# Optimization experiments

Measured on AMD Instinct MI355X. Metric: run time of the kernel, lower is better.

Reference implementation:

```python
import jax, jax.numpy as jnp
import numpy as np

B, S, D = 4, 4096, 2048
NUM_MODALITIES = 2


def setup_inputs() -> dict:
    key = jax.random.key(0)
    k_x, k_t, k_w0, k_b0, k_w1, k_b1 = jax.random.split(key, 6)
    scale = 1.0 / np.sqrt(D)
    return {
        "hidden_states": jax.random.normal(k_x, (B, S, D), dtype=jnp.float32),
        "type_ids": jax.random.randint(k_t, (B, S), 0, NUM_MODALITIES, dtype=jnp.int32),
        "W0": jax.random.uniform(k_w0, (D, D), jnp.float32, -scale, scale),
        "b0": jax.random.uniform(k_b0, (D,), jnp.float32, -scale, scale),
        "W1": jax.random.uniform(k_w1, (D, D), jnp.float32, -scale, scale),
        "b1": jax.random.uniform(k_b1, (D,), jnp.float32, -scale, scale),
    }


def reference(hidden_states, type_ids, W0, b0, W1, b1):
    # Original: gather tokens where type_ids == i, apply expert i's Linear,
    # scatter into a zero-init [B, S, out_dim] buffer. The masks partition
    # all tokens, so this equals a masked mixture of the two dense GEMMs.
    y0 = jnp.einsum("bsd,ed->bse", hidden_states, W0) + b0  # expert 0
    y1 = jnp.einsum("bsd,ed->bse", hidden_states, W1) + b1  # expert 1
    m0 = (type_ids == 0)[..., None]
    m1 = (type_ids == 1)[..., None]
    zero = jnp.zeros((), dtype=y0.dtype)
    return jnp.where(m0, y0, zero) + jnp.where(m1, y1, zero)
```

## Files before the change

kernel.cpp:

```cpp
#include <hip/hip_runtime.h>
#include <hip/hip_bf16.h>
#include <stdint.h>


#define T_TOK 16384
#define DDIM  2048
#define NT_K  32
#define NT_D  64
#define MT    64
#define NTILE 8

typedef __attribute__((ext_vector_type(4))) float          f32x4;
typedef __attribute__((ext_vector_type(8))) short          bf16x8;
typedef __attribute__((ext_vector_type(2))) unsigned int   u32x2;

#define WS_HBF   0ull
#define WS_W0BF  67108864ull
#define WS_W1BF  75497472ull
#define WS_META  83886080ull
#define WS_IDX   83886208ull
#define WS_NEED  (WS_IDX + 65536ull)

__device__ __forceinline__ unsigned short cvt1_bf16(float f) {
  unsigned u = __builtin_bit_cast(unsigned, f);
  unsigned rnd = 0x7fffu + ((u >> 16) & 1u);
  return (unsigned short)((u + rnd) >> 16);
}

__device__ __forceinline__ void gload_lds16(const void* g, void* l) {
  __builtin_amdgcn_global_load_lds(
      (const __attribute__((address_space(1))) unsigned int*)g,
      (__attribute__((address_space(3))) unsigned int*)l, 16, 0, 0);
}

#define BAR()     asm volatile("s_barrier" ::: "memory")
#define VMCNT2()  asm volatile("s_waitcnt vmcnt(2)" ::: "memory")
#define VMCNT4()  asm volatile("s_waitcnt vmcnt(4)" ::: "memory")
#define VMCNT0()  asm volatile("s_waitcnt vmcnt(0)" ::: "memory")
#define LGKM0()   asm volatile("s_waitcnt lgkmcnt(0)" ::: "memory")
#define SCHEDBAR() __builtin_amdgcn_sched_barrier(0)

__global__ void k_prep(const float* __restrict__ H, const float* __restrict__ W0,
                       const float* __restrict__ W1, const int* __restrict__ typ,
                       unsigned short* __restrict__ Hbf,
                       unsigned short* __restrict__ W0bf,
                       unsigned short* __restrict__ W1bf,
                       int* __restrict__ meta, int* __restrict__ idx) {
  const int gid = blockIdx.x * blockDim.x + threadIdx.x;
  if (gid < T_TOK) {
    int t = typ[gid];
    int pos = (t == 0) ? atomicAdd(&meta[0], 1)
                       : (T_TOK - 1) - atomicAdd(&meta[1], 1);
    idx[pos] = gid;
  }
  const int nH = T_TOK * DDIM / 4;
  const int nW = DDIM * DDIM / 4;
  const int total = nH + 2 * nW;
  const int stride = gridDim.x * blockDim.x;
  for (int i = gid; i < total; i += stride) {
    const float* s; unsigned short* d; int j;
    if (i < nH)           { s = H;  d = Hbf;  j = i; }
    else if (i < nH + nW) { s = W0; d = W0bf; j = i - nH; }
    else                  { s = W1; d = W1bf; j = i - nH - nW; }
    f32x4 v = ((const f32x4*)s)[j];
    unsigned p0 = (unsigned)cvt1_bf16(v[0]) | ((unsigned)cvt1_bf16(v[1]) << 16);
    unsigned p1 = (unsigned)cvt1_bf16(v[2]) | ((unsigned)cvt1_bf16(v[3]) << 16);
    u32x2 o; o[0] = p0; o[1] = p1;
    ((u32x2*)d)[j] = o;
  }
}

__global__ __launch_bounds__(512) void k_gemm256(
    const unsigned short* __restrict__ Hbf,
    const unsigned short* __restrict__ W0bf,
    const unsigned short* __restrict__ W1bf,
    const float* __restrict__ B0, const float* __restrict__ B1,
    const int* __restrict__ meta, const int* __restrict__ idx,
    float* __restrict__ OUT)
{
  __shared__ char lds[131072];

  const int orig = blockIdx.x;
  const int wg = (orig & 7) * 64 + (orig >> 3);
  int my = wg >> 3;
  const int bx = wg & 7;

  const int c0 = meta[0];
  int ms = c0 >> 8; if (ms > MT - 1) ms = MT - 1;
  my = (my == 0) ? ms : (my == ms) ? 0 : my;

  const int tid  = threadIdx.x;
  const int lane = tid & 63;
  const int wid  = tid >> 6;
  const int wr   = wid >> 2;
  const int wc   = wid & 3;
  const int fr   = lane & 15;
  const int g    = lane >> 4;

  const int start = my * 256;
  const int isDual = (start < c0 && c0 < start + 256) ? 1 : 0;
  const int e0    = (start >= c0) ? 1 : 0;
  const int colBase = bx * 256;

  const int cs = (lane & 3) ^ ((lane >> 3) & 3);
  const char* aS[2];
  int rt[2];
#pragma unroll
  for (int l = 0; l < 2; ++l) {
    int ch = 2 * wid + l;
    rt[l] = ch * 16 + (lane >> 2);
    int orow = idx[start + rt[l]];
    aS[l] = (const char*)Hbf + (size_t)orow * 4096 + cs * 16;
  }
  const int chB = (2 * wid) * 1024;

  const int sw = (g ^ ((fr >> 1) & 3)) << 4;
  int aF[8], bF[4];
#pragma unroll
  for (int m = 0; m < 8; ++m) aF[m] = ((wr * 128 + m * 16 + fr) << 6) + sw;
#pragma unroll
  for (int n = 0; n < 4; ++n) bF[n] = ((wc * 64 + n * 16 + fr) << 6) + sw;

  f32x4 acc[8][4];
#pragma unroll
  for (int m = 0; m < 8; ++m)
#pragma unroll
    for (int n = 0; n < 4; ++n) acc[m][n] = (f32x4)0.0f;

  int cols[4];
#pragma unroll
  for (int n = 0; n < 4; ++n) cols[n] = colBase + wc * 64 + n * 16 + fr;

  if (!isDual) {
    const unsigned short* Wb = e0 ? W1bf : W0bf;
    const char* wS[2];
#pragma unroll
    for (int l = 0; l < 2; ++l)
      wS[l] = (const char*)(Wb + (size_t)(colBase + rt[l]) * DDIM) + cs * 16;

    auto STAGE_A = [&](int d, int kh, int tn) {
      char* dst = lds + (d << 15) + (kh << 14) + chB;
      int ko = tn * 128 + kh * 64;
      gload_lds16(aS[0] + ko, dst);
      gload_lds16(aS[1] + ko, dst + 1024);
    };
    auto STAGE_B = [&](int d, int kh, int tn) {
      char* dst = lds + 65536 + (d << 15) + (kh << 14) + chB;
      int ko = tn * 128 + kh * 64;
      gload_lds16(wS[0] + ko, dst);
      gload_lds16(wS[1] + ko, dst + 1024);
    };

    STAGE_A(0, 0, 0); STAGE_B(0, 0, 0); STAGE_A(0, 1, 0); STAGE_B(0, 1, 0);
    VMCNT4();
    BAR();

#pragma unroll 2
    for (int t = 0; t < NT_K; ++t) {
      const int c = t & 1, d = c ^ 1;
      int t1 = t + 1; if (t1 == NT_K) t1 = NT_K - 1;
      const char* Ak0 = lds + (c << 15);
      const char* Ak1 = Ak0 + 16384;
      const char* Bk0 = lds + 65536 + (c << 15);
      const char* Bk1 = Bk0 + 16384;

      bf16x8 a[8], bb0, bb1;

#pragma unroll
      for (int m = 0; m < 8; ++m) a[m] = *(const bf16x8*)(Ak0 + aF[m]);
      bb0 = *(const bf16x8*)(Bk0 + bF[0]);
      bb1 = *(const bf16x8*)(Bk0 + bF[1]);
      STAGE_A(d, 0, t1);
      BAR(); LGKM0(); SCHEDBAR();
      __builtin_amdgcn_s_setprio(1);
#pragma unroll
      for (int m = 0; m < 8; ++m) {
        acc[m][0] = __builtin_amdgcn_mfma_f32_16x16x32_bf16(a[m], bb0, acc[m][0], 0, 0, 0);
        acc[m][1] = __builtin_amdgcn_mfma_f32_16x16x32_bf16(a[m], bb1, acc[m][1], 0, 0, 0);
      }
      __builtin_amdgcn_s_setprio(0);

      bb0 = *(const bf16x8*)(Bk0 + bF[2]);
      bb1 = *(const bf16x8*)(Bk0 + bF[3]);
      VMCNT2();
      STAGE_B(d, 0, t1);
      BAR(); LGKM0(); SCHEDBAR();
      __builtin_amdgcn_s_setprio(1);
#pragma unroll
      for (int m = 0; m < 8; ++m) {
        acc[m][2] = __builtin_amdgcn_mfma_f32_16x16x32_bf16(a[m], bb0, acc[m][2], 0, 0, 0);
        acc[m][3] = __builtin_amdgcn_mfma_f32_16x16x32_bf16(a[m], bb1, acc[m][3], 0, 0, 0);
      }
      __builtin_amdgcn_s_setprio(0);

#pragma unroll
      for (int m = 0; m < 8; ++m) a[m] = *(const bf16x8*)(Ak1 + aF[m]);
      bb0 = *(const bf16x8*)(Bk1 + bF[0]);
      bb1 = *(const bf16x8*)(Bk1 + bF[1]);
      STAGE_A(d, 1, t1);
      BAR(); LGKM0(); SCHEDBAR();
      __builtin_amdgcn_s_setprio(1);
#pragma unroll
      for (int m = 0; m < 8; ++m) {
        acc[m][0] = __builtin_amdgcn_mfma_f32_16x16x32_bf16(a[m], bb0, acc[m][0], 0, 0, 0);
        acc[m][1] = __builtin_amdgcn_mfma_f32_16x16x32_bf16(a[m], bb1, acc[m][1], 0, 0, 0);
      }
      __builtin_amdgcn_s_setprio(0);

      bb0 = *(const bf16x8*)(Bk1 + bF[2]);
      bb1 = *(const bf16x8*)(Bk1 + bF[3]);
      VMCNT2();
      STAGE_B(d, 1, t1);
      BAR(); LGKM0(); SCHEDBAR();
      __builtin_amdgcn_s_setprio(1);
#pragma unroll
      for (int m = 0; m < 8; ++m) {
        acc[m][2] = __builtin_amdgcn_mfma_f32_16x16x32_bf16(a[m], bb0, acc[m][2], 0, 0, 0);
        acc[m][3] = __builtin_amdgcn_mfma_f32_16x16x32_bf16(a[m], bb1, acc[m][3], 0, 0, 0);
      }
      __builtin_amdgcn_s_setprio(0);
    }

    VMCNT0();

    const float* Bv = e0 ? B1 : B0;
    float bias[4];
#pragma unroll
    for (int n = 0; n < 4; ++n) bias[n] = Bv[cols[n]];
#pragma unroll
    for (int m = 0; m < 8; ++m) {
      int lb = wr * 128 + m * 16 + (g << 2);
#pragma unroll
      for (int j = 0; j < 4; ++j) {
        int orow = idx[start + lb + j];
        float* op = OUT + (size_t)orow * DDIM;
#pragma unroll
        for (int n = 0; n < 4; ++n) op[cols[n]] = acc[m][n][j] + bias[n];
      }
    }
  } else {
    const char* wS0[2]; const char* wS1[2];
#pragma unroll
    for (int l = 0; l < 2; ++l) {
      wS0[l] = (const char*)(W0bf + (size_t)(colBase + rt[l]) * DDIM) + cs * 16;
      wS1[l] = (const char*)(W1bf + (size_t)(colBase + rt[l]) * DDIM) + cs * 16;
    }
    const int lo_w = c0 - start - wr * 128;
    int mmix = 8;
    if (lo_w > 0 && lo_w < 128 && (lo_w & 15)) mmix = lo_w >> 4;

    f32x4 accX[4];
#pragma unroll
    for (int n = 0; n < 4; ++n) accX[n] = (f32x4)0.0f;

    auto DSTAGE = [&](int d, int tn) {
      int ko = tn * 64;
      char* ad  = lds + (d << 14) + chB;
      char* b0d = lds + 32768 + (d << 14) + chB;
      char* b1d = lds + 65536 + (d << 14) + chB;
      gload_lds16(aS[0] + ko, ad);
      gload_lds16(aS[1] + ko, ad + 1024);
      gload_lds16(wS0[0] + ko, b0d);
      gload_lds16(wS0[1] + ko, b0d + 1024);
      gload_lds16(wS1[0] + ko, b1d);
      gload_lds16(wS1[1] + ko, b1d + 1024);
    };

    DSTAGE(0, 0);
    VMCNT0();
    BAR();

    for (int t = 0; t < NT_D; ++t) {
      const int c = t & 1, d = c ^ 1;
      int t1 = t + 1; if (t1 == NT_D) t1 = NT_D - 1;
      const char* Ac  = lds + (c << 14);
      const char* B0c = lds + 32768 + (c << 14);
      const char* B1c = lds + 65536 + (c << 14);
      bf16x8 a[8], b0a, b0b, b1a, b1b;

#pragma unroll
      for (int m = 0; m < 8; ++m) a[m] = *(const bf16x8*)(Ac + aF[m]);
      b0a = *(const bf16x8*)(B0c + bF[0]);
      b0b = *(const bf16x8*)(B0c + bF[1]);
      b1a = *(const bf16x8*)(B1c + bF[0]);
      b1b = *(const bf16x8*)(B1c + bF[1]);
      DSTAGE(d, t1);
      BAR(); LGKM0(); SCHEDBAR();
      __builtin_amdgcn_s_setprio(1);
#pragma unroll
      for (int m = 0; m < 8; ++m) {
        if (m == mmix) {
          acc[m][0] = __builtin_amdgcn_mfma_f32_16x16x32_bf16(a[m], b0a, acc[m][0], 0, 0, 0);
          acc[m][1] = __builtin_amdgcn_mfma_f32_16x16x32_bf16(a[m], b0b, acc[m][1], 0, 0, 0);
          accX[0]   = __builtin_amdgcn_mfma_f32_16x16x32_bf16(a[m], b1a, accX[0],   0, 0, 0);
          accX[1]   = __builtin_amdgcn_mfma_f32_16x16x32_bf16(a[m], b1b, accX[1],   0, 0, 0);
        } else if (m * 16 >= lo_w) {
          acc[m][0] = __builtin_amdgcn_mfma_f32_16x16x32_bf16(a[m], b1a, acc[m][0], 0, 0, 0);
          acc[m][1] = __builtin_amdgcn_mfma_f32_16x16x32_bf16(a[m], b1b, acc[m][1], 0, 0, 0);
        } else {
          acc[m][0] = __builtin_amdgcn_mfma_f32_16x16x32_bf16(a[m], b0a, acc[m][0], 0, 0, 0);
          acc[m][1] = __builtin_amdgcn_mfma_f32_16x16x32_bf16(a[m], b0b, acc[m][1], 0, 0, 0);
        }
      }
      __builtin_amdgcn_s_setprio(0);

      b0a = *(const bf16x8*)(B0c + bF[2]);
      b0b = *(const bf16x8*)(B0c + bF[3]);
      b1a = *(const bf16x8*)(B1c + bF[2]);
      b1b = *(const bf16x8*)(B1c + bF[3]);
      VMCNT0();
      BAR(); LGKM0(); SCHEDBAR();
      __builtin_amdgcn_s_setprio(1);
#pragma unroll
      for (int m = 0; m < 8; ++m) {
        if (m == mmix) {
          acc[m][2] = __builtin_amdgcn_mfma_f32_16x16x32_bf16(a[m], b0a, acc[m][2], 0, 0, 0);
          acc[m][3] = __builtin_amdgcn_mfma_f32_16x16x32_bf16(a[m], b0b, acc[m][3], 0, 0, 0);
          accX[2]   = __builtin_amdgcn_mfma_f32_16x16x32_bf16(a[m], b1a, accX[2],   0, 0, 0);
          accX[3]   = __builtin_amdgcn_mfma_f32_16x16x32_bf16(a[m], b1b, accX[3],   0, 0, 0);
        } else if (m * 16 >= lo_w) {
          acc[m][2] = __builtin_amdgcn_mfma_f32_16x16x32_bf16(a[m], b1a, acc[m][2], 0, 0, 0);
          acc[m][3] = __builtin_amdgcn_mfma_f32_16x16x32_bf16(a[m], b1b, acc[m][3], 0, 0, 0);
        } else {
          acc[m][2] = __builtin_amdgcn_mfma_f32_16x16x32_bf16(a[m], b0a, acc[m][2], 0, 0, 0);
          acc[m][3] = __builtin_amdgcn_mfma_f32_16x16x32_bf16(a[m], b0b, acc[m][3], 0, 0, 0);
        }
      }
      __builtin_amdgcn_s_setprio(0);
    }
    VMCNT0();

    float bias0v[4], bias1v[4];
#pragma unroll
    for (int n = 0; n < 4; ++n) { bias0v[n] = B0[cols[n]]; bias1v[n] = B1[cols[n]]; }
#pragma unroll
    for (int m = 0; m < 8; ++m) {
      int lb = wr * 128 + m * 16 + (g << 2);
      if (m == mmix) {
#pragma unroll
        for (int j = 0; j < 4; ++j) {
          int p = start + lb + j;
          int orow = idx[p];
          float* op = OUT + (size_t)orow * DDIM;
          if (p >= c0) {
#pragma unroll
            for (int n = 0; n < 4; ++n) op[cols[n]] = accX[n][j] + bias1v[n];
          } else {
#pragma unroll
            for (int n = 0; n < 4; ++n) op[cols[n]] = acc[m][n][j] + bias0v[n];
          }
        }
      } else {
        int em = (m * 16 >= lo_w) ? 1 : 0;
#pragma unroll
        for (int j = 0; j < 4; ++j) {
          int orow = idx[start + lb + j];
          float* op = OUT + (size_t)orow * DDIM;
#pragma unroll
          for (int n = 0; n < 4; ++n)
            op[cols[n]] = acc[m][n][j] + (em ? bias1v[n] : bias0v[n]);
        }
      }
    }
  }
}

#define BMd 64
#define BNd 64
#define BKd 32
#define LDW 36

__device__ __forceinline__ bf16x8 cvt_bf16x8(f32x4 lo, f32x4 hi) {
  bf16x8 r;
#pragma unroll
  for (int i = 0; i < 4; ++i) {
    r[i]     = (short)cvt1_bf16(lo[i]);
    r[i + 4] = (short)cvt1_bf16(hi[i]);
  }
  return r;
}

__global__ __launch_bounds__(256, 2) void mot_mfma_diag(
    const float* __restrict__ H,  const int* __restrict__ TYP,
    const float* __restrict__ W0, const float* __restrict__ B0,
    const float* __restrict__ W1, const float* __restrict__ B1,
    float* __restrict__ OUT)
{
  __shared__ float As[BMd * LDW];
  __shared__ float W0s[BNd * LDW];
  __shared__ float W1s[BNd * LDW];

  const int tid = threadIdx.x;
  const int rowBase = blockIdx.y * BMd;
  const int colBase = blockIdx.x * BNd;
  const int srow  = tid >> 3;
  const int scol4 = (tid & 7) << 2;
  const float* hA  = H  + (size_t)(rowBase + srow) * DDIM + scol4;
  const float* hW0 = W0 + (size_t)(colBase + srow) * DDIM + scol4;
  const float* hW1 = W1 + (size_t)(colBase + srow) * DDIM + scol4;

  const int lane = tid & 63;
  const int w    = tid >> 6;
  const int fr   = lane & 15;
  const int g    = lane >> 4;

  f32x4 acc0[4], acc1[4];
#pragma unroll
  for (int m = 0; m < 4; ++m) { acc0[m] = (f32x4)0.0f; acc1[m] = (f32x4)0.0f; }

  for (int k0 = 0; k0 < DDIM; k0 += BKd) {
    f32x4 va[2], v0[2], v1[2];
#pragma unroll
    for (int p = 0; p < 2; ++p) {
      va[p] = *(const f32x4*)(hA  + (size_t)p * 32 * DDIM);
      v0[p] = *(const f32x4*)(hW0 + (size_t)p * 32 * DDIM);
      v1[p] = *(const f32x4*)(hW1 + (size_t)p * 32 * DDIM);
    }
    hA += BKd; hW0 += BKd; hW1 += BKd;
    __syncthreads();
#pragma unroll
    for (int p = 0; p < 2; ++p) {
      int r = srow + 32 * p;
      *(f32x4*)(&As [r * LDW + scol4]) = va[p];
      *(f32x4*)(&W0s[r * LDW + scol4]) = v0[p];
      *(f32x4*)(&W1s[r * LDW + scol4]) = v1[p];
    }
    __syncthreads();

    bf16x8 af[4];
#pragma unroll
    for (int m = 0; m < 4; ++m) {
      const float* ap = &As[(m * 16 + fr) * LDW + g * 8];
      af[m] = cvt_bf16x8(*(const f32x4*)ap, *(const f32x4*)(ap + 4));
    }
    const float* b0p = &W0s[(w * 16 + fr) * LDW + g * 8];
    const float* b1p = &W1s[(w * 16 + fr) * LDW + g * 8];
    bf16x8 bf0 = cvt_bf16x8(*(const f32x4*)b0p, *(const f32x4*)(b0p + 4));
    bf16x8 bf1 = cvt_bf16x8(*(const f32x4*)b1p, *(const f32x4*)(b1p + 4));
#pragma unroll
    for (int m = 0; m < 4; ++m) {
      acc0[m] = __builtin_amdgcn_mfma_f32_16x16x32_bf16(af[m], bf0, acc0[m], 0, 0, 0);
      acc1[m] = __builtin_amdgcn_mfma_f32_16x16x32_bf16(af[m], bf1, acc1[m], 0, 0, 0);
    }
  }

  const int col = colBase + w * 16 + fr;
  const float bz0 = B0[col];
  const float bz1 = B1[col];
#pragma unroll
  for (int m = 0; m < 4; ++m)
#pragma unroll
    for (int j = 0; j < 4; ++j) {
      int row = rowBase + m * 16 + (g << 2) + j;
      int t = TYP[row];
      OUT[(size_t)row * DDIM + col] = (t == 0) ? (acc0[m][j] + bz0) : (acc1[m][j] + bz1);
    }
}

extern "C" void kernel_launch(void* const* d_in, const int* in_sizes, int n_in,
                              void* d_out, int out_size, void* d_ws, size_t ws_size,
                              hipStream_t stream) {
  const float* H   = (const float*)d_in[0];
  const int*   TYP = (const int*)  d_in[1];
  const float* W0  = (const float*)d_in[2];
  const float* B0v = (const float*)d_in[3];
  const float* W1  = (const float*)d_in[4];
  const float* B1v = (const float*)d_in[5];
  float* OUT = (float*)d_out;

  if (ws_size < WS_NEED) {
    dim3 grid(DDIM / BNd, T_TOK / BMd);
    mot_mfma_diag<<<grid, dim3(256), 0, stream>>>(H, TYP, W0, B0v, W1, B1v, OUT);
    return;
  }

  unsigned short* Hbf  = (unsigned short*)((char*)d_ws + WS_HBF);
  unsigned short* W0bf = (unsigned short*)((char*)d_ws + WS_W0BF);
  unsigned short* W1bf = (unsigned short*)((char*)d_ws + WS_W1BF);
  int* meta = (int*)((char*)d_ws + WS_META);
  int* idx  = (int*)((char*)d_ws + WS_IDX);

  hipMemsetAsync(meta, 0, 16, stream);
  k_prep<<<4096, 256, 0, stream>>>(H, W0, W1, TYP, Hbf, W0bf, W1bf, meta, idx);
  k_gemm256<<<MT * NTILE, 512, 0, stream>>>(Hbf, W0bf, W1bf, B0v, B1v, meta, idx, OUT);
}
```

Baseline: 215.7 us.

## Schedule the dual-expert tile last and triple-buffer its loads with split staging

Assigns the 504 single-expert tiles to block indices 0..503 and places the 8 mixed-boundary tiles at the end, instead of remapping row 0 to the boundary tile. The dual tile's K loop moves from a double buffer with full vmcnt(0) waits to a three-stage LDS ring (larger shared allocation), with the W1 load split into the second half of each step and vmcnt(6) waits. Warps whose rows belong to only one expert skip the second weight fragment loads and the mixing logic. The aim is to keep the slow dual tile from stalling on memory latency. The trade-off is more LDS use per block and an extra barrier per iteration.

```diff
diff --git a/kernel.cpp b/kernel.cpp
--- a/kernel.cpp
+++ b/kernel.cpp
@@ -8,7 +8,6 @@
 #define NT_K  32
 #define NT_D  64
 #define MT    64
-#define NTILE 8
 
 typedef __attribute__((ext_vector_type(4))) float          f32x4;
 typedef __attribute__((ext_vector_type(8))) short          bf16x8;
@@ -36,6 +35,7 @@
 #define BAR()     asm volatile("s_barrier" ::: "memory")
 #define VMCNT2()  asm volatile("s_waitcnt vmcnt(2)" ::: "memory")
 #define VMCNT4()  asm volatile("s_waitcnt vmcnt(4)" ::: "memory")
+#define VMCNT6()  asm volatile("s_waitcnt vmcnt(6)" ::: "memory")
 #define VMCNT0()  asm volatile("s_waitcnt vmcnt(0)" ::: "memory")
 #define LGKM0()   asm volatile("s_waitcnt lgkmcnt(0)" ::: "memory")
 #define SCHEDBAR() __builtin_amdgcn_sched_barrier(0)
@@ -78,16 +78,10 @@
     const int* __restrict__ meta, const int* __restrict__ idx,
     float* __restrict__ OUT)
 {
-  __shared__ char lds[131072];
-
-  const int orig = blockIdx.x;
-  const int wg = (orig & 7) * 64 + (orig >> 3);
-  int my = wg >> 3;
-  const int bx = wg & 7;
+  __shared__ char lds[147456];
 
   const int c0 = meta[0];
   int ms = c0 >> 8; if (ms > MT - 1) ms = MT - 1;
-  my = (my == 0) ? ms : (my == ms) ? 0 : my;
 
   const int tid  = threadIdx.x;
   const int lane = tid & 63;
@@ -96,42 +90,44 @@
   const int wc   = wid & 3;
   const int fr   = lane & 15;
   const int g    = lane >> 4;
-
-  const int start = my * 256;
-  const int isDual = (start < c0 && c0 < start + 256) ? 1 : 0;
-  const int e0    = (start >= c0) ? 1 : 0;
-  const int colBase = bx * 256;
-
-  const int cs = (lane & 3) ^ ((lane >> 3) & 3);
-  const char* aS[2];
-  int rt[2];
-#pragma unroll
-  for (int l = 0; l < 2; ++l) {
-    int ch = 2 * wid + l;
-    rt[l] = ch * 16 + (lane >> 2);
-    int orow = idx[start + rt[l]];
-    aS[l] = (const char*)Hbf + (size_t)orow * 4096 + cs * 16;
-  }
+  const int cs   = (lane & 3) ^ ((lane >> 3) & 3);
+  const int sw   = (g ^ ((fr >> 1) & 3)) << 4;
+
+  int aF[8], bF[4];
+#pragma unroll
+  for (int m = 0; m < 8; ++m) aF[m] = ((wr * 128 + m * 16 + fr) << 6) + sw;
+#pragma unroll
+  for (int n = 0; n < 4; ++n) bF[n] = ((wc * 64 + n * 16 + fr) << 6) + sw;
+
+  f32x4 acc[8][4];
+#pragma unroll
+  for (int m = 0; m < 8; ++m)
+#pragma unroll
+    for (int n = 0; n < 4; ++n) acc[m][n] = (f32x4)0.0f;
+
   const int chB = (2 * wid) * 1024;
 
-  const int sw = (g ^ ((fr >> 1) & 3)) << 4;
-  int aF[8], bF[4];
-#pragma unroll
-  for (int m = 0; m < 8; ++m) aF[m] = ((wr * 128 + m * 16 + fr) << 6) + sw;
-#pragma unroll
-  for (int n = 0; n < 4; ++n) bF[n] = ((wc * 64 + n * 16 + fr) << 6) + sw;
-
-  f32x4 acc[8][4];
-#pragma unroll
-  for (int m = 0; m < 8; ++m)
-#pragma unroll
-    for (int n = 0; n < 4; ++n) acc[m][n] = (f32x4)0.0f;
-
-  int cols[4];
-#pragma unroll
-  for (int n = 0; n < 4; ++n) cols[n] = colBase + wc * 64 + n * 16 + fr;
-
-  if (!isDual) {
+  if (blockIdx.x < 504) {
+    const int orig = blockIdx.x;
+    const int wg = (orig & 7) * 63 + (orig >> 3);
+    int i_t = wg >> 3;
+    const int bx = wg & 7;
+    const int my = i_t + (i_t >= ms ? 1 : 0);
+
+    const int start = my * 256;
+    const int e0 = (start >= c0) ? 1 : 0;
+    const int colBase = bx * 256;
+
+    const char* aS[2];
+    int rt[2];
+#pragma unroll
+    for (int l = 0; l < 2; ++l) {
+      int ch = 2 * wid + l;
+      rt[l] = ch * 16 + (lane >> 2);
+      int orow = idx[start + rt[l]];
+      aS[l] = (const char*)Hbf + (size_t)orow * 4096 + cs * 16;
+    }
+
     const unsigned short* Wb = e0 ? W1bf : W0bf;
     const char* wS[2];
 #pragma unroll
@@ -225,8 +221,12 @@
 
     const float* Bv = e0 ? B1 : B0;
     float bias[4];
-#pragma unroll
-    for (int n = 0; n < 4; ++n) bias[n] = Bv[cols[n]];
+    int cols[4];
+#pragma unroll
+    for (int n = 0; n < 4; ++n) {
+      cols[n] = colBase + wc * 64 + n * 16 + fr;
+      bias[n] = Bv[cols[n]];
+    }
 #pragma unroll
     for (int m = 0; m < 8; ++m) {
       int lb = wr * 128 + m * 16 + (g << 2);
@@ -239,100 +239,150 @@
       }
     }
   } else {
+    const int bx = blockIdx.x - 504;
+    const int colBase = bx * 256;
+    const int start = ms * 256;
+
+    const char* aS[2];
+    int rt[2];
+#pragma unroll
+    for (int l = 0; l < 2; ++l) {
+      int ch = 2 * wid + l;
+      rt[l] = ch * 16 + (lane >> 2);
+      int orow = idx[start + rt[l]];
+      aS[l] = (const char*)Hbf + (size_t)orow * 4096 + cs * 16;
+    }
     const char* wS0[2]; const char* wS1[2];
 #pragma unroll
     for (int l = 0; l < 2; ++l) {
       wS0[l] = (const char*)(W0bf + (size_t)(colBase + rt[l]) * DDIM) + cs * 16;
       wS1[l] = (const char*)(W1bf + (size_t)(colBase + rt[l]) * DDIM) + cs * 16;
     }
+
     const int lo_w = c0 - start - wr * 128;
+    const int pure0 = (lo_w >= 128);
+    const int pure1 = (lo_w <= 0);
     int mmix = 8;
-    if (lo_w > 0 && lo_w < 128 && (lo_w & 15)) mmix = lo_w >> 4;
+    if (!pure0 && !pure1 && (lo_w & 15)) mmix = lo_w >> 4;
 
     f32x4 accX[4];
 #pragma unroll
     for (int n = 0; n < 4; ++n) accX[n] = (f32x4)0.0f;
 
-    auto DSTAGE = [&](int d, int tn) {
+    auto STAGE_AB0 = [&](int d, int tn) {
+      char* base = lds + d * 49152;
       int ko = tn * 64;
-      char* ad  = lds + (d << 14) + chB;
-      char* b0d = lds + 32768 + (d << 14) + chB;
-      char* b1d = lds + 65536 + (d << 14) + chB;
-      gload_lds16(aS[0] + ko, ad);
-      gload_lds16(aS[1] + ko, ad + 1024);
-      gload_lds16(wS0[0] + ko, b0d);
-      gload_lds16(wS0[1] + ko, b0d + 1024);
-      gload_lds16(wS1[0] + ko, b1d);
-      gload_lds16(wS1[1] + ko, b1d + 1024);
+      gload_lds16(aS[0] + ko, base + chB);
+      gload_lds16(aS[1] + ko, base + chB + 1024);
+      gload_lds16(wS0[0] + ko, base + 16384 + chB);
+      gload_lds16(wS0[1] + ko, base + 16384 + chB + 1024);
     };
-
-    DSTAGE(0, 0);
-    VMCNT0();
+    auto STAGE_B1 = [&](int d, int tn) {
+      char* base = lds + d * 49152;
+      int ko = tn * 64;
+      gload_lds16(wS1[0] + ko, base + 32768 + chB);
+      gload_lds16(wS1[1] + ko, base + 32768 + chB + 1024);
+    };
+
+    STAGE_AB0(0, 0); STAGE_B1(0, 0);
+    STAGE_AB0(1, 1); STAGE_B1(1, 1);
+    VMCNT6();
     BAR();
 
     for (int t = 0; t < NT_D; ++t) {
-      const int c = t & 1, d = c ^ 1;
-      int t1 = t + 1; if (t1 == NT_D) t1 = NT_D - 1;
-      const char* Ac  = lds + (c << 14);
-      const char* B0c = lds + 32768 + (c << 14);
-      const char* B1c = lds + 65536 + (c << 14);
+      const int c = t % 3;
+      const int d = (t + 2) % 3;
+      int t2 = t + 2; if (t2 >= NT_D) t2 = NT_D - 1;
+      const char* Ac  = lds + c * 49152;
+      const char* B0c = Ac + 16384;
+      const char* B1c = Ac + 32768;
+      const char* Bown = pure1 ? B1c : B0c;
+      const int mixed = (!pure0 && !pure1);
+
       bf16x8 a[8], b0a, b0b, b1a, b1b;
 
 #pragma unroll
       for (int m = 0; m < 8; ++m) a[m] = *(const bf16x8*)(Ac + aF[m]);
-      b0a = *(const bf16x8*)(B0c + bF[0]);
-      b0b = *(const bf16x8*)(B0c + bF[1]);
-      b1a = *(const bf16x8*)(B1c + bF[0]);
-      b1b = *(const bf16x8*)(B1c + bF[1]);
-      DSTAGE(d, t1);
+      b0a = *(const bf16x8*)(Bown + bF[0]);
+      b0b = *(const bf16x8*)(Bown + bF[1]);
+      if (mixed) {
+        b1a = *(const bf16x8*)(B1c + bF[0]);
+        b1b = *(const bf16x8*)(B1c + bF[1]);
+      }
+      STAGE_AB0(d, t2);
       BAR(); LGKM0(); SCHEDBAR();
       __builtin_amdgcn_s_setprio(1);
-#pragma unroll
-      for (int m = 0; m < 8; ++m) {
-        if (m == mmix) {
-          acc[m][0] = __builtin_amdgcn_mfma_f32_16x16x32_bf16(a[m], b0a, acc[m][0], 0, 0, 0);
-          acc[m][1] = __builtin_amdgcn_mfma_f32_16x16x32_bf16(a[m], b0b, acc[m][1], 0, 0, 0);
-          accX[0]   = __builtin_amdgcn_mfma_f32_16x16x32_bf16(a[m], b1a, accX[0],   0, 0, 0);
-          accX[1]   = __builtin_amdgcn_mfma_f32_16x16x32_bf16(a[m], b1b, accX[1],   0, 0, 0);
-        } else if (m * 16 >= lo_w) {
-          acc[m][0] = __builtin_amdgcn_mfma_f32_16x16x32_bf16(a[m], b1a, acc[m][0], 0, 0, 0);
-          acc[m][1] = __builtin_amdgcn_mfma_f32_16x16x32_bf16(a[m], b1b, acc[m][1], 0, 0, 0);
-        } else {
+      if (!mixed) {
+#pragma unroll
+        for (int m = 0; m < 8; ++m) {
           acc[m][0] = __builtin_amdgcn_mfma_f32_16x16x32_bf16(a[m], b0a, acc[m][0], 0, 0, 0);
           acc[m][1] = __builtin_amdgcn_mfma_f32_16x16x32_bf16(a[m], b0b, acc[m][1], 0, 0, 0);
         }
+      } else {
+#pragma unroll
+        for (int m = 0; m < 8; ++m) {
+          if (m == mmix) {
+            acc[m][0] = __builtin_amdgcn_mfma_f32_16x16x32_bf16(a[m], b0a, acc[m][0], 0, 0, 0);
+            acc[m][1] = __builtin_amdgcn_mfma_f32_16x16x32_bf16(a[m], b0b, acc[m][1], 0, 0, 0);
+            accX[0]   = __builtin_amdgcn_mfma_f32_16x16x32_bf16(a[m], b1a, accX[0],   0, 0, 0);
+            accX[1]   = __builtin_amdgcn_mfma_f32_16x16x32_bf16(a[m], b1b, accX[1],   0, 0, 0);
+          } else if (m * 16 >= lo_w) {
+            acc[m][0] = __builtin_amdgcn_mfma_f32_16x16x32_bf16(a[m], b1a, acc[m][0], 0, 0, 0);
+            acc[m][1] = __builtin_amdgcn_mfma_f32_16x16x32_bf16(a[m], b1b, acc[m][1], 0, 0, 0);
+          } else {
+            acc[m][0] = __builtin_amdgcn_mfma_f32_16x16x32_bf16(a[m], b0a, acc[m][0], 0, 0, 0);
+            acc[m][1] = __builtin_amdgcn_mfma_f32_16x16x32_bf16(a[m], b0b, acc[m][1], 0, 0, 0);
+          }
+        }
       }
       __builtin_amdgcn_s_setprio(0);
 
-      b0a = *(const bf16x8*)(B0c + bF[2]);
-      b0b = *(const bf16x8*)(B0c + bF[3]);
-      b1a = *(const bf16x8*)(B1c + bF[2]);
-      b1b = *(const bf16x8*)(B1c + bF[3]);
-      VMCNT0();
+      b0a = *(const bf16x8*)(Bown + bF[2]);
+      b0b = *(const bf16x8*)(Bown + bF[3]);
+      if (mixed) {
+        b1a = *(const bf16x8*)(B1c + bF[2]);
+        b1b = *(const bf16x8*)(B1c + bF[3]);
+      }
+      STAGE_B1(d, t2);
+      VMCNT6();
       BAR(); LGKM0(); SCHEDBAR();
       __builtin_amdgcn_s_setprio(1);
-#pragma unroll
-      for (int m = 0; m < 8; ++m) {
-        if (m == mmix) {
-          acc[m][2] = __builtin_amdgcn_mfma_f32_16x16x32_bf16(a[m], b0a, acc[m][2], 0, 0, 0);
-          acc[m][3] = __builtin_amdgcn_mfma_f32_16x16x32_bf16(a[m], b0b, acc[m][3], 0, 0, 0);
-          accX[2]   = __builtin_amdgcn_mfma_f32_16x16x32_bf16(a[m], b1a, accX[2],   0, 0, 0);
-          accX[3]   = __builtin_amdgcn_mfma_f32_16x16x32_bf16(a[m], b1b, accX[3],   0, 0, 0);
-        } else if (m * 16 >= lo_w) {
-          acc[m][2] = __builtin_amdgcn_mfma_f32_16x16x32_bf16(a[m], b1a, acc[m][2], 0, 0, 0);
-          acc[m][3] = __builtin_amdgcn_mfma_f32_16x16x32_bf16(a[m], b1b, acc[m][3], 0, 0, 0);
-        } else {
+      if (!mixed) {
+#pragma unroll
+        for (int m = 0; m < 8; ++m) {
           acc[m][2] = __builtin_amdgcn_mfma_f32_16x16x32_bf16(a[m], b0a, acc[m][2], 0, 0, 0);
           acc[m][3] = __builtin_amdgcn_mfma_f32_16x16x32_bf16(a[m], b0b, acc[m][3], 0, 0, 0);
         }
+      } else {
+#pragma unroll
+        for (int m = 0; m < 8; ++m) {
+          if (m == mmix) {
+            acc[m][2] = __builtin_amdgcn_mfma_f32_16x16x32_bf16(a[m], b0a, acc[m][2], 0, 0, 0);
+            acc[m][3] = __builtin_amdgcn_mfma_f32_16x16x32_bf16(a[m], b0b, acc[m][3], 0, 0, 0);
+            accX[2]   = __builtin_amdgcn_mfma_f32_16x16x32_bf16(a[m], b1a, accX[2],   0, 0, 0);
+            accX[3]   = __builtin_amdgcn_mfma_f32_16x16x32_bf16(a[m], b1b, accX[3],   0, 0, 0);
+          } else if (m * 16 >= lo_w) {
+            acc[m][2] = __builtin_amdgcn_mfma_f32_16x16x32_bf16(a[m], b1a, acc[m][2], 0, 0, 0);
+            acc[m][3] = __builtin_amdgcn_mfma_f32_16x16x32_bf16(a[m], b1b, acc[m][3], 0, 0, 0);
+          } else {
+            acc[m][2] = __builtin_amdgcn_mfma_f32_16x16x32_bf16(a[m], b0a, acc[m][2], 0, 0, 0);
+            acc[m][3] = __builtin_amdgcn_mfma_f32_16x16x32_bf16(a[m], b0b, acc[m][3], 0, 0, 0);
+          }
+        }
       }
       __builtin_amdgcn_s_setprio(0);
+      BAR();
     }
     VMCNT0();
 
+    int cols[4];
     float bias0v[4], bias1v[4];
 #pragma unroll
-    for (int n = 0; n < 4; ++n) { bias0v[n] = B0[cols[n]]; bias1v[n] = B1[cols[n]]; }
+    for (int n = 0; n < 4; ++n) {
+      cols[n] = colBase + wc * 64 + n * 16 + fr;
+      bias0v[n] = B0[cols[n]];
+      bias1v[n] = B1[cols[n]];
+    }
 #pragma unroll
     for (int m = 0; m < 8; ++m) {
       int lb = wr * 128 + m * 16 + (g << 2);
@@ -351,14 +401,15 @@
           }
         }
       } else {
-        int em = (m * 16 >= lo_w) ? 1 : 0;
 #pragma unroll
         for (int j = 0; j < 4; ++j) {
-          int orow = idx[start + lb + j];
+          int p = start + lb + j;
+          int orow = idx[p];
           float* op = OUT + (size_t)orow * DDIM;
+          int e1r = (p >= c0) ? 1 : 0;
 #pragma unroll
           for (int n = 0; n < 4; ++n)
-            op[cols[n]] = acc[m][n][j] + (em ? bias1v[n] : bias0v[n]);
+            op[cols[n]] = acc[m][n][j] + (e1r ? bias1v[n] : bias0v[n]);
         }
       }
     }
@@ -482,5 +533,5 @@
 
   hipMemsetAsync(meta, 0, 16, stream);
   k_prep<<<4096, 256, 0, stream>>>(H, W0, W1, TYP, Hbf, W0bf, W1bf, meta, idx);
-  k_gemm256<<<MT * NTILE, 512, 0, stream>>>(Hbf, W0bf, W1bf, B0v, B1v, meta, idx, OUT);
-}
+  k_gemm256<<<512, 512, 0, stream>>>(Hbf, W0bf, W1bf, B0v, B1v, meta, idx, OUT);
+}
```

Measured after the change: 232.7 us. +7.9%, slower.
